# Performance work log

Hardware: AMD Instinct MI355X
Metric: run time of the kernel (lower is better)

The kernel has to match this reference:

```python
import jax, jax.numpy as jnp
import numpy as np

NX, NC = 8192, 8192
X_DIM, C_DIM, H_DIM, K_DIM, Y_DIM = 3, 3, 512, 512, 3
N_LAYERS = 4
ACTIVATION = 'sigmoid'


def _init_mlp(key, in_dim, h_dim, out_dim, n_layers):
    ks = jax.random.split(key, 3)
    W0 = jax.random.normal(ks[0], (in_dim, h_dim), jnp.float32) / np.sqrt(in_dim)
    b0 = jnp.zeros((h_dim,), jnp.float32)
    Wh = jax.random.normal(ks[1], (n_layers - 1, h_dim, h_dim), jnp.float32) / np.sqrt(h_dim)
    bh = jnp.zeros((n_layers - 1, h_dim), jnp.float32)
    Wo = jax.random.normal(ks[2], (h_dim, out_dim), jnp.float32) / np.sqrt(h_dim)
    bo = jnp.zeros((out_dim,), jnp.float32)
    return W0, b0, Wh, bh, Wo, bo


def _mlp(x, W0, b0, Wh, bh, Wo, bo):
    # SIREN-style MLP (BaseNet with x_scale=alpha=gamma=1)
    h = jnp.sin(x @ W0 + b0)
    for i in range(Wh.shape[0]):  # fixed small n_layers-1 loop
        h = jnp.sin(h @ Wh[i] + bh[i])
    return h @ Wo + bo


def setup_inputs() -> dict:
    key = jax.random.key(0)
    kx, kc, kq, kk, kv = jax.random.split(key, 5)
    inp = {
        'x': jax.random.normal(kx, (NX, X_DIM), jnp.float32),
        'c': jax.random.normal(kc, (NC, C_DIM), jnp.float32),
    }
    for name, k, in_dim, out_dim in (('Q', kq, X_DIM, K_DIM), ('K', kk, C_DIM, K_DIM), ('V', kv, C_DIM, Y_DIM)):
        W0, b0, Wh, bh, Wo, bo = _init_mlp(k, in_dim, H_DIM, out_dim, N_LAYERS)
        inp[f'{name}W0'], inp[f'{name}b0'] = W0, b0
        inp[f'{name}Wh'], inp[f'{name}bh'] = Wh, bh
        inp[f'{name}Wo'], inp[f'{name}bo'] = Wo, bo
    return inp


def reference(x, c, QW0, Qb0, QWh, Qbh, QWo, Qbo,
              KW0, Kb0, KWh, Kbh, KWo, Kbo,
              VW0, Vb0, VWh, Vbh, VWo, Vbo):
    Q = _mlp(x, QW0, Qb0, QWh, Qbh, QWo, Qbo)   # [Nx, k_dim]
    K = _mlp(c, KW0, Kb0, KWh, Kbh, KWo, Kbo)   # [Nc, k_dim]
    V = _mlp(c, VW0, Vb0, VWh, Vbh, VWo, Vbo)   # [Nc, y_dim]
    A = Q @ K.T                                  # [Nx, Nc]
    if ACTIVATION == 'sigmoid':
        A = jax.nn.sigmoid(A)
    elif ACTIVATION == 'softplus':
        A = jax.nn.softplus(A)
    elif ACTIVATION == 'softmax':
        A = jax.nn.softmax(A, axis=1)
    return A @ V                                 # [Nx, y_dim]
```

## Files before the change

kernel.cpp:

```cpp
#include <hip/hip_runtime.h>
#include <math.h>

#define NXR 8192
#define NCR 8192
#define HD  512
#define NSL 8
#define JC  (NCR / NSL)
#define KSTR 520

typedef short s16x8 __attribute__((ext_vector_type(8)));
typedef float f32x4 __attribute__((ext_vector_type(4)));
typedef unsigned short u16;

struct P11 { const float* p[11]; };
struct P3  { const float* p[3]; };

__device__ inline u16 f2bf(float f) {
    unsigned int u = __float_as_uint(f);
    u = (u + 0x7FFFu + ((u >> 16) & 1u)) >> 16;
    return (u16)u;
}
__device__ inline float bf2f(u16 h) {
    return __uint_as_float(((unsigned int)h) << 16);
}

__device__ inline void async_load16(const void* g, void* l) {
    __builtin_amdgcn_global_load_lds(
        (const __attribute__((address_space(1))) unsigned int*)g,
        (__attribute__((address_space(3))) unsigned int*)l, 16, 0, 0);
}

__global__ __launch_bounds__(256) void transpose_w_all(
    P11 srcs, u16* __restrict__ out)
{
    const float* in = srcs.p[blockIdx.z];
    u16* o = out + (size_t)blockIdx.z * HD * HD;
    __shared__ float tile[32][33];
    int bx = blockIdx.x * 32, by = blockIdx.y * 32;
    int tx = threadIdx.x & 31, ty = threadIdx.x >> 5;
    for (int r = ty; r < 32; r += 8)
        tile[r][tx] = in[(size_t)(by + r) * HD + bx + tx];
    __syncthreads();
    for (int r = ty; r < 32; r += 8)
        o[(size_t)(bx + r) * HD + by + tx] = f2bf(tile[tx][r]);
}

__global__ __launch_bounds__(256) void layer0_all(
    const float* __restrict__ x, const float* __restrict__ c,
    P3 W0p, P3 b0p, u16* __restrict__ H)
{
    int z = blockIdx.z;
    const float* X  = (z == 0) ? x : c;
    const float* W0 = W0p.p[z];
    const float* b0 = b0p.p[z];
    u16* Hn = H + (size_t)z * NXR * HD;

    int idx = (blockIdx.x * 256 + threadIdx.x) * 8;
    int n = idx & (HD - 1);
    int row = idx >> 9;
    float x0 = X[row * 3 + 0], x1 = X[row * 3 + 1], x2 = X[row * 3 + 2];
    s16x8 o;
#pragma unroll
    for (int j = 0; j < 8; ++j) {
        float v = x0 * W0[n + j] + x1 * W0[HD + n + j] + x2 * W0[2 * HD + n + j] + b0[n + j];
        ((u16*)&o)[j] = f2bf(__sinf(v));
    }
    *(s16x8*)&Hn[idx] = o;
}

template<int ACT>
__global__ __launch_bounds__(256) void gemm_rs(
    const u16* __restrict__ Abase, const u16* __restrict__ Wt0, size_t wstride,
    P3 bias, u16* __restrict__ Cbase)
{
    __shared__ u16 Ws[2][32 * KSTR];

    const int net = blockIdx.z;
    const u16* A  = Abase + (size_t)net * NXR * HD;
    const u16* Wt = Wt0 + (size_t)net * wstride;
    const float* bias_p = bias.p[net];
    u16* C = Cbase + (size_t)net * NXR * HD;

    const int tid = threadIdx.x;
    const int wave = tid >> 6, lane = tid & 63;
    const int row0 = blockIdx.x * 128;
    const int colbase = blockIdx.y * 128;

    const int qm = lane & 15;
    const int g  = lane >> 4;

#pragma unroll
    for (int i = 0; i < 8; ++i) {
        int cc = i * 4 + wave;
        async_load16(Wt + (size_t)(colbase + cc) * HD + lane * 8,
                     &Ws[0][cc * KSTR + lane * 8]);
    }

    s16x8 qf[16][2];
    {
        const u16* ap = A + (size_t)(row0 + wave * 32 + qm) * HD + g * 8;
#pragma unroll
        for (int t = 0; t < 16; ++t) {
            qf[t][0] = *(const s16x8*)(ap + t * 32);
            qf[t][1] = *(const s16x8*)(ap + (size_t)16 * HD + t * 32);
        }
    }
    __syncthreads();

    int p = 0;
#pragma unroll 1
    for (int ct = 0; ct < 4; ++ct) {
        const int col0 = colbase + ct * 32;

        if (ct + 1 < 4) {
#pragma unroll
            for (int i = 0; i < 8; ++i) {
                int cc = i * 4 + wave;
                async_load16(Wt + (size_t)(colbase + (ct + 1) * 32 + cc) * HD + lane * 8,
                             &Ws[p ^ 1][cc * KSTR + lane * 8]);
            }
        }

        const u16* Wb = Ws[p];
        f32x4 acc[2][2] = {};
#pragma unroll
        for (int kt = 0; kt < 16; ++kt) {
            s16x8 b0 = *(const s16x8*)&Wb[qm * KSTR + kt * 32 + g * 8];
            s16x8 b1 = *(const s16x8*)&Wb[(16 + qm) * KSTR + kt * 32 + g * 8];
            acc[0][0] = __builtin_amdgcn_mfma_f32_16x16x32_bf16(qf[kt][0], b0, acc[0][0], 0, 0, 0);
            acc[0][1] = __builtin_amdgcn_mfma_f32_16x16x32_bf16(qf[kt][0], b1, acc[0][1], 0, 0, 0);
            acc[1][0] = __builtin_amdgcn_mfma_f32_16x16x32_bf16(qf[kt][1], b0, acc[1][0], 0, 0, 0);
            acc[1][1] = __builtin_amdgcn_mfma_f32_16x16x32_bf16(qf[kt][1], b1, acc[1][1], 0, 0, 0);
        }

        float bv0 = bias_p[col0 + qm];
        float bv1 = bias_p[col0 + 16 + qm];
#pragma unroll
        for (int hh = 0; hh < 2; ++hh) {
#pragma unroll
            for (int r = 0; r < 4; ++r) {
                int grow = row0 + wave * 32 + hh * 16 + g * 4 + r;
                float v0 = acc[hh][0][r] + bv0;
                float v1 = acc[hh][1][r] + bv1;
                if (ACT) { v0 = __sinf(v0); v1 = __sinf(v1); }
                C[(size_t)grow * HD + col0 + qm]      = f2bf(v0);
                C[(size_t)grow * HD + col0 + 16 + qm] = f2bf(v1);
            }
        }
        __syncthreads();
        p ^= 1;
    }
}

__global__ __launch_bounds__(256) void vout_k(
    const u16* __restrict__ H, const float* __restrict__ Wo,
    const float* __restrict__ bo, float* __restrict__ V)
{
    int wave = threadIdx.x >> 6, lane = threadIdx.x & 63;
    int row = blockIdx.x * 4 + wave;
    s16x8 hv = *(const s16x8*)(H + (size_t)row * HD + lane * 8);
    float a0 = 0, a1 = 0, a2 = 0;
#pragma unroll
    for (int j = 0; j < 8; ++j) {
        float hf = bf2f(((const u16*)&hv)[j]);
        int k = lane * 8 + j;
        a0 += hf * Wo[k * 3 + 0];
        a1 += hf * Wo[k * 3 + 1];
        a2 += hf * Wo[k * 3 + 2];
    }
#pragma unroll
    for (int d = 32; d >= 1; d >>= 1) {
        a0 += __shfl_down(a0, d);
        a1 += __shfl_down(a1, d);
        a2 += __shfl_down(a2, d);
    }
    if (lane == 0) {
        V[row * 3 + 0] = a0 + bo[0];
        V[row * 3 + 1] = a1 + bo[1];
        V[row * 3 + 2] = a2 + bo[2];
    }
}

__global__ __launch_bounds__(256) void attn_mfma(
    const u16* __restrict__ Q, const u16* __restrict__ K,
    const float* __restrict__ V, float* __restrict__ out)
{
    __shared__ u16 Ks[2][32 * KSTR];

    const int tid = threadIdx.x;
    const int wave = tid >> 6, lane = tid & 63;
    const int row0 = blockIdx.y * 128;
    const int col_base = blockIdx.x * JC;

    const int qm = lane & 15;
    const int g  = lane >> 4;

#pragma unroll
    for (int i = 0; i < 8; ++i) {
        int cc = i * 4 + wave;
        async_load16(K + (size_t)(col_base + cc) * HD + lane * 8,
                     &Ks[0][cc * KSTR + lane * 8]);
    }

    s16x8 qf[16][2];
    {
        const u16* qp = Q + (size_t)(row0 + wave * 32 + qm) * HD + g * 8;
#pragma unroll
        for (int t = 0; t < 16; ++t) {
            qf[t][0] = *(const s16x8*)(qp + t * 32);
            qf[t][1] = *(const s16x8*)(qp + (size_t)16 * HD + t * 32);
        }
    }
    __syncthreads();

    float po[2][4][3] = {};
    int p = 0;

#pragma unroll 1
    for (int jt = 0; jt < JC / 32; ++jt) {
        const int col0 = col_base + jt * 32;

        if (jt + 1 < JC / 32) {
#pragma unroll
            for (int i = 0; i < 8; ++i) {
                int cc = i * 4 + wave;
                async_load16(K + (size_t)(col0 + 32 + cc) * HD + lane * 8,
                             &Ks[p ^ 1][cc * KSTR + lane * 8]);
            }
        }

        float vv[2][3];
#pragma unroll
        for (int ct = 0; ct < 2; ++ct) {
            size_t vr = (size_t)(col0 + ct * 16 + qm) * 3;
            vv[ct][0] = V[vr + 0];
            vv[ct][1] = V[vr + 1];
            vv[ct][2] = V[vr + 2];
        }

        const u16* Kb = Ks[p];
        f32x4 acc[2][2] = {};
#pragma unroll
        for (int kt = 0; kt < 16; ++kt) {
            s16x8 b0 = *(const s16x8*)&Kb[qm * KSTR + kt * 32 + g * 8];
            s16x8 b1 = *(const s16x8*)&Kb[(16 + qm) * KSTR + kt * 32 + g * 8];
            acc[0][0] = __builtin_amdgcn_mfma_f32_16x16x32_bf16(qf[kt][0], b0, acc[0][0], 0, 0, 0);
            acc[0][1] = __builtin_amdgcn_mfma_f32_16x16x32_bf16(qf[kt][0], b1, acc[0][1], 0, 0, 0);
            acc[1][0] = __builtin_amdgcn_mfma_f32_16x16x32_bf16(qf[kt][1], b0, acc[1][0], 0, 0, 0);
            acc[1][1] = __builtin_amdgcn_mfma_f32_16x16x32_bf16(qf[kt][1], b1, acc[1][1], 0, 0, 0);
        }

#pragma unroll
        for (int h = 0; h < 2; ++h)
#pragma unroll
            for (int ct = 0; ct < 2; ++ct)
#pragma unroll
                for (int r = 0; r < 4; ++r) {
                    float s = __builtin_amdgcn_rcpf(1.f + __expf(-acc[h][ct][r]));
                    po[h][r][0] += s * vv[ct][0];
                    po[h][r][1] += s * vv[ct][1];
                    po[h][r][2] += s * vv[ct][2];
                }
        __syncthreads();
        p ^= 1;
    }

#pragma unroll
    for (int h = 0; h < 2; ++h)
#pragma unroll
        for (int r = 0; r < 4; ++r)
#pragma unroll
            for (int c = 0; c < 3; ++c) {
                float v = po[h][r][c];
                v += __shfl_down(v, 8, 16);
                v += __shfl_down(v, 4, 16);
                v += __shfl_down(v, 2, 16);
                v += __shfl_down(v, 1, 16);
                if (qm == 0)
                    atomicAdd(&out[(size_t)(row0 + wave * 32 + h * 16 + g * 4 + r) * 3 + c], v);
            }
}

extern "C" void kernel_launch(void* const* d_in, const int* in_sizes, int n_in,
                              void* d_out, int out_size, void* d_ws, size_t ws_size,
                              hipStream_t stream)
{
    const float* x   = (const float*)d_in[0];
    const float* c   = (const float*)d_in[1];
    const float* QW0 = (const float*)d_in[2];
    const float* Qb0 = (const float*)d_in[3];
    const float* QWh = (const float*)d_in[4];
    const float* Qbh = (const float*)d_in[5];
    const float* QWo = (const float*)d_in[6];
    const float* Qbo = (const float*)d_in[7];
    const float* KW0 = (const float*)d_in[8];
    const float* Kb0 = (const float*)d_in[9];
    const float* KWh = (const float*)d_in[10];
    const float* Kbh = (const float*)d_in[11];
    const float* KWo = (const float*)d_in[12];
    const float* Kbo = (const float*)d_in[13];
    const float* VW0 = (const float*)d_in[14];
    const float* Vb0 = (const float*)d_in[15];
    const float* VWh = (const float*)d_in[16];
    const float* Vbh = (const float*)d_in[17];
    const float* VWo = (const float*)d_in[18];
    const float* Vbo = (const float*)d_in[19];

    char* ws = (char*)d_ws;
    const size_t WTN = (size_t)HD * HD;
    const size_t NET = (size_t)NXR * HD;

    u16*   wT = (u16*)ws;
    u16*   hA = (u16*)(ws + 11 * WTN * sizeof(u16));
    u16*   hB = hA;
    float* Vf = (float*)(ws + 11 * WTN * sizeof(u16) + 3 * NET * sizeof(u16));

    u16* hA2 = (u16*)(ws + 11 * WTN * sizeof(u16));
    u16* hB2 = (u16*)(ws + 11 * WTN * sizeof(u16) + 3 * NET * sizeof(u16));
    Vf = (float*)(ws + 11 * WTN * sizeof(u16) + 6 * NET * sizeof(u16));

    P11 tsrc;
    for (int l = 0; l < 3; ++l) {
        tsrc.p[l * 3 + 0] = QWh + (size_t)l * WTN;
        tsrc.p[l * 3 + 1] = KWh + (size_t)l * WTN;
        tsrc.p[l * 3 + 2] = VWh + (size_t)l * WTN;
    }
    tsrc.p[9]  = QWo;
    tsrc.p[10] = KWo;
    transpose_w_all<<<dim3(16, 16, 11), 256, 0, stream>>>(tsrc, wT);

    {
        P3 w0 = {{QW0, KW0, VW0}}, b0 = {{Qb0, Kb0, Vb0}};
        layer0_all<<<dim3(NXR * HD / 2048, 1, 3), 256, 0, stream>>>(x, c, w0, b0, hA2);
    }

    dim3 g3(NXR / 128, HD / 128, 3);
    {
        P3 b = {{Qbh + 0 * HD, Kbh + 0 * HD, Vbh + 0 * HD}};
        gemm_rs<1><<<g3, 256, 0, stream>>>(hA2, wT + 0 * 3 * WTN, WTN, b, hB2);
    }
    {
        P3 b = {{Qbh + 1 * HD, Kbh + 1 * HD, Vbh + 1 * HD}};
        gemm_rs<1><<<g3, 256, 0, stream>>>(hB2, wT + 1 * 3 * WTN, WTN, b, hA2);
    }
    {
        P3 b = {{Qbh + 2 * HD, Kbh + 2 * HD, Vbh + 2 * HD}};
        gemm_rs<1><<<g3, 256, 0, stream>>>(hA2, wT + 2 * 3 * WTN, WTN, b, hB2);
    }
    {
        P3 b = {{Qbo, Kbo, nullptr}};
        gemm_rs<0><<<dim3(NXR / 128, HD / 128, 2), 256, 0, stream>>>(
            hB2, wT + 9 * WTN, WTN, b, hA2);
    }
    vout_k<<<NCR / 4, 256, 0, stream>>>(hB2 + 2 * NET, VWo, Vbo, Vf);

    hipMemsetAsync(d_out, 0, (size_t)out_size * sizeof(float), stream);
    attn_mfma<<<dim3(NSL, NXR / 128), 256, 0, stream>>>(
        hA2, hA2 + NET, Vf, (float*)d_out);
}
```

Baseline: 291.0 us.

## Reshape hidden-layer GEMM tiles to 64x256 with 128-thread blocks and single-buffered LDS

The hidden-layer GEMM kernel now uses 2 waves per block, each tile covering 64 rows by 256 columns, with each wave still keeping 32 rows of A in registers. LDS weight staging drops from a double buffer to a single buffer, and the next column chunk is loaded only after a barrier. The intent is to halve LDS use and raise occupancy while reusing each A register fragment across more columns. In exchange, the weight-load latency is no longer overlapped with MFMA work, and there is an extra barrier per column chunk.

```diff
diff --git a/kernel.cpp b/kernel.cpp
--- a/kernel.cpp
+++ b/kernel.cpp
@@ -69,11 +69,11 @@
 }
 
 template<int ACT>
-__global__ __launch_bounds__(256) void gemm_rs(
+__global__ __launch_bounds__(128) void gemm_sm(
     const u16* __restrict__ Abase, const u16* __restrict__ Wt0, size_t wstride,
     P3 bias, u16* __restrict__ Cbase)
 {
-    __shared__ u16 Ws[2][32 * KSTR];
+    __shared__ u16 Ws[32 * KSTR];
 
     const int net = blockIdx.z;
     const u16* A  = Abase + (size_t)net * NXR * HD;
@@ -83,17 +83,17 @@
 
     const int tid = threadIdx.x;
     const int wave = tid >> 6, lane = tid & 63;
-    const int row0 = blockIdx.x * 128;
-    const int colbase = blockIdx.y * 128;
+    const int row0 = blockIdx.x * 64;
+    const int colbase = blockIdx.y * 256;
 
     const int qm = lane & 15;
     const int g  = lane >> 4;
 
 #pragma unroll
-    for (int i = 0; i < 8; ++i) {
-        int cc = i * 4 + wave;
+    for (int i = 0; i < 16; ++i) {
+        int cc = i * 2 + wave;
         async_load16(Wt + (size_t)(colbase + cc) * HD + lane * 8,
-                     &Ws[0][cc * KSTR + lane * 8]);
+                     &Ws[cc * KSTR + lane * 8]);
     }
 
     s16x8 qf[16][2];
@@ -107,30 +107,29 @@
     }
     __syncthreads();
 
-    int p = 0;
 #pragma unroll 1
-    for (int ct = 0; ct < 4; ++ct) {
+    for (int ct = 0; ct < 8; ++ct) {
         const int col0 = colbase + ct * 32;
 
-        if (ct + 1 < 4) {
-#pragma unroll
-            for (int i = 0; i < 8; ++i) {
-                int cc = i * 4 + wave;
-                async_load16(Wt + (size_t)(colbase + (ct + 1) * 32 + cc) * HD + lane * 8,
-                             &Ws[p ^ 1][cc * KSTR + lane * 8]);
-            }
-        }
-
-        const u16* Wb = Ws[p];
         f32x4 acc[2][2] = {};
 #pragma unroll
         for (int kt = 0; kt < 16; ++kt) {
-            s16x8 b0 = *(const s16x8*)&Wb[qm * KSTR + kt * 32 + g * 8];
-            s16x8 b1 = *(const s16x8*)&Wb[(16 + qm) * KSTR + kt * 32 + g * 8];
+            s16x8 b0 = *(const s16x8*)&Ws[qm * KSTR + kt * 32 + g * 8];
+            s16x8 b1 = *(const s16x8*)&Ws[(16 + qm) * KSTR + kt * 32 + g * 8];
             acc[0][0] = __builtin_amdgcn_mfma_f32_16x16x32_bf16(qf[kt][0], b0, acc[0][0], 0, 0, 0);
             acc[0][1] = __builtin_amdgcn_mfma_f32_16x16x32_bf16(qf[kt][0], b1, acc[0][1], 0, 0, 0);
             acc[1][0] = __builtin_amdgcn_mfma_f32_16x16x32_bf16(qf[kt][1], b0, acc[1][0], 0, 0, 0);
             acc[1][1] = __builtin_amdgcn_mfma_f32_16x16x32_bf16(qf[kt][1], b1, acc[1][1], 0, 0, 0);
+        }
+        __syncthreads();
+
+        if (ct + 1 < 8) {
+#pragma unroll
+            for (int i = 0; i < 16; ++i) {
+                int cc = i * 2 + wave;
+                async_load16(Wt + (size_t)(colbase + (ct + 1) * 32 + cc) * HD + lane * 8,
+                             &Ws[cc * KSTR + lane * 8]);
+            }
         }
 
         float bv0 = bias_p[col0 + qm];
@@ -148,7 +147,6 @@
             }
         }
         __syncthreads();
-        p ^= 1;
     }
 }
 
@@ -312,12 +310,8 @@
 
     u16*   wT = (u16*)ws;
     u16*   hA = (u16*)(ws + 11 * WTN * sizeof(u16));
-    u16*   hB = hA;
-    float* Vf = (float*)(ws + 11 * WTN * sizeof(u16) + 3 * NET * sizeof(u16));
-
-    u16* hA2 = (u16*)(ws + 11 * WTN * sizeof(u16));
-    u16* hB2 = (u16*)(ws + 11 * WTN * sizeof(u16) + 3 * NET * sizeof(u16));
-    Vf = (float*)(ws + 11 * WTN * sizeof(u16) + 6 * NET * sizeof(u16));
+    u16*   hB = (u16*)(ws + 11 * WTN * sizeof(u16) + 3 * NET * sizeof(u16));
+    float* Vf = (float*)(ws + 11 * WTN * sizeof(u16) + 6 * NET * sizeof(u16));
 
     P11 tsrc;
     for (int l = 0; l < 3; ++l) {
@@ -331,30 +325,30 @@
 
     {
         P3 w0 = {{QW0, KW0, VW0}}, b0 = {{Qb0, Kb0, Vb0}};
-        layer0_all<<<dim3(NXR * HD / 2048, 1, 3), 256, 0, stream>>>(x, c, w0, b0, hA2);
-    }
-
-    dim3 g3(NXR / 128, HD / 128, 3);
+        layer0_all<<<dim3(NXR * HD / 2048, 1, 3), 256, 0, stream>>>(x, c, w0, b0, hA);
+    }
+
+    dim3 g3(NXR / 64, HD / 256, 3);
     {
         P3 b = {{Qbh + 0 * HD, Kbh + 0 * HD, Vbh + 0 * HD}};
-        gemm_rs<1><<<g3, 256, 0, stream>>>(hA2, wT + 0 * 3 * WTN, WTN, b, hB2);
+        gemm_sm<1><<<g3, 128, 0, stream>>>(hA, wT + 0 * 3 * WTN, WTN, b, hB);
     }
     {
         P3 b = {{Qbh + 1 * HD, Kbh + 1 * HD, Vbh + 1 * HD}};
-        gemm_rs<1><<<g3, 256, 0, stream>>>(hB2, wT + 1 * 3 * WTN, WTN, b, hA2);
+        gemm_sm<1><<<g3, 128, 0, stream>>>(hB, wT + 1 * 3 * WTN, WTN, b, hA);
     }
     {
         P3 b = {{Qbh + 2 * HD, Kbh + 2 * HD, Vbh + 2 * HD}};
-        gemm_rs<1><<<g3, 256, 0, stream>>>(hA2, wT + 2 * 3 * WTN, WTN, b, hB2);
+        gemm_sm<1><<<g3, 128, 0, stream>>>(hA, wT + 2 * 3 * WTN, WTN, b, hB);
     }
     {
         P3 b = {{Qbo, Kbo, nullptr}};
-        gemm_rs<0><<<dim3(NXR / 128, HD / 128, 2), 256, 0, stream>>>(
-            hB2, wT + 9 * WTN, WTN, b, hA2);
-    }
-    vout_k<<<NCR / 4, 256, 0, stream>>>(hB2 + 2 * NET, VWo, Vbo, Vf);
+        gemm_sm<0><<<dim3(NXR / 64, HD / 256, 2), 128, 0, stream>>>(
+            hB, wT + 9 * WTN, WTN, b, hA);
+    }
+    vout_k<<<NCR / 4, 256, 0, stream>>>(hB + 2 * NET, VWo, Vbo, Vf);
 
     hipMemsetAsync(d_out, 0, (size_t)out_size * sizeof(float), stream);
     attn_mfma<<<dim3(NSL, NXR / 128), 256, 0, stream>>>(
-        hA2, hA2 + NET, Vf, (float*)d_out);
-}
+        hA, hA + NET, Vf, (float*)d_out);
+}
```

Result: no change. 288.2 us (-1.0%).
